# Kernel tuning notes

Measured on AMD Instinct MI355X. Metric: run time of the kernel, lower is better.

## Reference

```python
import jax, jax.numpy as jnp
import numpy as np

T, B, C = 2048, 8, 1024
H, K, PAD_L = 16, 31, 30
G = C // H


def setup_inputs() -> dict:
    key = jax.random.key(0)
    k1, k2 = jax.random.split(key)
    x = jax.random.normal(k1, (T, B, C), dtype=jnp.float32)
    # xavier_uniform for weight of shape (H, 1, K): fan_in=K, fan_out=H*... torch treats
    # dims as (out=H, in=1, receptive=K) -> fan_in=1*K, fan_out=H? Actually torch computes
    # fan_in = 1*K, fan_out = H*K for a (H,1,K) tensor is not right; torch: fan_in = in*rf = 1*K,
    # fan_out = out*rf = H*K? No: for (H,1,K), fan_in = 1*K, fan_out = H*K / H? Use standard formula:
    # fan_in = size(1)*K = K, fan_out = size(0)*K = H*K -> bound = sqrt(6/(K + H*K))
    bound = float(np.sqrt(6.0 / (K + H * K)))
    weight = jax.random.uniform(k2, (H, 1, K), dtype=jnp.float32, minval=-bound, maxval=bound)
    bias = jnp.zeros((C,), dtype=jnp.float32)
    return {"x": x, "weight": weight, "bias": bias}


def reference(x, weight, bias):
    # x: [T, B, C]; weight: [H, 1, K]; bias: [C]
    w = jax.nn.softmax(weight, axis=-1)  # per-head softmax over kernel taps
    # expand head weights to per-channel depthwise kernel: [C, 1, K]
    w_ch = jnp.repeat(w, G, axis=0)  # each of the G channels in head h shares w[h]
    xb = jnp.transpose(x, (1, 2, 0))  # [B, C, T]
    out = jax.lax.conv_general_dilated(
        xb, w_ch,
        window_strides=(1,),
        padding=[(PAD_L, 0)],  # left (causal) padding
        dimension_numbers=("NCH", "OIH", "NCH"),
        feature_group_count=C,
    )  # [B, C, T]
    out = jnp.transpose(out, (2, 0, 1))  # [T, B, C]
    return out + bias
```

## Files before the change

kernel.cpp:

```cpp
#include <hip/hip_runtime.h>
#include <hip/hip_bf16.h>

constexpr int T = 2048;
constexpr int B = 8;
constexpr int C = 1024;
constexpr int H = 16;
constexpr int K = 31;
constexpr int BC = B * C;

constexpr int TT = 32;
constexpr int NB = K - 1 + TT;
constexpr int BLOCK = 256;
constexpr int BLK_PER_CHUNK = BC / BLOCK;
constexpr int NCHUNK = T / TT;
constexpr int NBLK = BLK_PER_CHUNK * NCHUNK;

__global__ __launch_bounds__(BLOCK, 4) void lconv_tbc_kernel(
        const float* __restrict__ x,
        const float* __restrict__ w,
        const float* __restrict__ bias,
        float* __restrict__ out) {
    const int tid = threadIdx.x;
    const int cb = blockIdx.x & (BLK_PER_CHUNK - 1);
    const int chunk = blockIdx.x / BLK_PER_CHUNK;
    const int bc = cb * BLOCK + tid;
    const int c = bc & (C - 1);
    const int h = __builtin_amdgcn_readfirstlane(c >> 6);

    float wv[K];
    float m = -1e30f;
    #pragma unroll
    for (int k = 0; k < K; ++k) {
        wv[k] = w[h * K + k];
        m = fmaxf(m, wv[k]);
    }
    float s = 0.0f;
    #pragma unroll
    for (int k = 0; k < K; ++k) {
        wv[k] = __expf(wv[k] - m);
        s += wv[k];
    }
    const float inv = 1.0f / s;
    float wr[K];
    #pragma unroll
    for (int d = 0; d < K; ++d)
        wr[d] = __uint_as_float(
            __builtin_amdgcn_readfirstlane(__float_as_uint(wv[K - 1 - d] * inv)));

    const float bi = bias[c];
    const int t0 = chunk * TT;
    const int base = t0 * BC + bc;

    float buf[NB];
    if (chunk == 0) {
        #pragma unroll
        for (int j = 0; j < K - 1; ++j) buf[j] = 0.0f;
    } else {
        #pragma unroll
        for (int j = 0; j < K - 1; ++j)
            buf[j] = x[base + (j - (K - 1)) * BC];
    }
    #pragma unroll
    for (int u = 0; u < TT; ++u)
        buf[K - 1 + u] = x[base + u * BC];

    #pragma unroll
    for (int u = 0; u < TT; ++u) {
        float acc = bi;
        #pragma unroll
        for (int d = 0; d < K; ++d)
            acc = fmaf(wr[d], buf[K - 1 + u - d], acc);
        __builtin_nontemporal_store(acc, &out[base + u * BC]);
    }
}

extern "C" void kernel_launch(void* const* d_in, const int* in_sizes, int n_in,
                              void* d_out, int out_size, void* d_ws, size_t ws_size,
                              hipStream_t stream) {
    const float* x = (const float*)d_in[0];
    const float* w = (const float*)d_in[1];
    const float* bias = (const float*)d_in[2];
    float* out = (float*)d_out;

    lconv_tbc_kernel<<<dim3(NBLK), dim3(BLOCK), 0, stream>>>(x, w, bias, out);
}
```

Before: 29.97 us.

## Stage input tile into LDS via async global_load_lds before convolution

Replaces the per-thread scalar global loads of the 61-row time window with wave-cooperative 16-byte global_load_lds transfers into a shared tile, overlapped with the softmax weight computation, then reads rows from LDS into registers after a barrier. It aims to cut the number of memory instructions and hide load latency behind the softmax. In exchange it adds about 61KB of LDS per block plus a block-wide sync, and lowers the launch-bounds occupancy hint from 4 to 2.

```diff
diff --git a/kernel.cpp b/kernel.cpp
--- a/kernel.cpp
+++ b/kernel.cpp
@@ -1,5 +1,5 @@
 #include <hip/hip_runtime.h>
-#include <hip/hip_bf16.h>
+#include <stdint.h>
 
 constexpr int T = 2048;
 constexpr int B = 8;
@@ -9,23 +9,44 @@
 constexpr int BC = B * C;
 
 constexpr int TT = 32;
-constexpr int NB = K - 1 + TT;
+constexpr int NR = K - 1 + TT;
 constexpr int BLOCK = 256;
 constexpr int BLK_PER_CHUNK = BC / BLOCK;
 constexpr int NCHUNK = T / TT;
 constexpr int NBLK = BLK_PER_CHUNK * NCHUNK;
 
-__global__ __launch_bounds__(BLOCK, 4) void lconv_tbc_kernel(
+typedef const __attribute__((address_space(1))) uint32_t gas_u32;
+typedef __attribute__((address_space(3))) uint32_t las_u32;
+
+__global__ __launch_bounds__(BLOCK, 2) void lconv_tbc_kernel(
         const float* __restrict__ x,
         const float* __restrict__ w,
         const float* __restrict__ bias,
         float* __restrict__ out) {
+    __shared__ float tile[NR][BLOCK];
+
     const int tid = threadIdx.x;
+    const int wid = tid >> 6;
+    const int lane = tid & 63;
     const int cb = blockIdx.x & (BLK_PER_CHUNK - 1);
     const int chunk = blockIdx.x / BLK_PER_CHUNK;
-    const int bc = cb * BLOCK + tid;
+    const int bc0 = cb * BLOCK;
+    const int bc = bc0 + tid;
     const int c = bc & (C - 1);
     const int h = __builtin_amdgcn_readfirstlane(c >> 6);
+    const int t0 = chunk * TT;
+
+    for (int r = wid; r < NR; r += 4) {
+        const int tg = t0 - (K - 1) + r;
+        if (tg >= 0) {
+            const float* src = x + (size_t)tg * BC + bc0 + lane * 4;
+            __builtin_amdgcn_global_load_lds(
+                (gas_u32*)src, (las_u32*)&tile[r][lane * 4], 16, 0, 0);
+        } else {
+            float4 z = {0.f, 0.f, 0.f, 0.f};
+            *(float4*)&tile[r][lane * 4] = z;
+        }
+    }
 
     float wv[K];
     float m = -1e30f;
@@ -46,24 +67,15 @@
     for (int d = 0; d < K; ++d)
         wr[d] = __uint_as_float(
             __builtin_amdgcn_readfirstlane(__float_as_uint(wv[K - 1 - d] * inv)));
+    const float bi = bias[c];
 
-    const float bi = bias[c];
-    const int t0 = chunk * TT;
+    __syncthreads();
+
+    float buf[NR];
+    #pragma unroll
+    for (int r = 0; r < NR; ++r) buf[r] = tile[r][tid];
+
     const int base = t0 * BC + bc;
-
-    float buf[NB];
-    if (chunk == 0) {
-        #pragma unroll
-        for (int j = 0; j < K - 1; ++j) buf[j] = 0.0f;
-    } else {
-        #pragma unroll
-        for (int j = 0; j < K - 1; ++j)
-            buf[j] = x[base + (j - (K - 1)) * BC];
-    }
-    #pragma unroll
-    for (int u = 0; u < TT; ++u)
-        buf[K - 1 + u] = x[base + u * BC];
-
     #pragma unroll
     for (int u = 0; u < TT; ++u) {
         float acc = bi;
```

Measured after the change: 31.32 us. +4.5%, slower.

## Double-buffer input chunks via async global-to-LDS loads with register halo reuse

Applied to the files above, without the earlier changes.

Each block now processes a 64-step time segment in four 16-step chunks. The next chunk is streamed into a double-buffered LDS area with global_load_lds DMA while the current chunk is computed, and hand-written vmcnt waits sequence the two. The 30-step halo is carried in registers between chunks, which cuts the redundant halo reloads of the old one-chunk-per-block scheme from about 1x to about 0.5x of the input. In exchange it relies on fragile hard-coded vmcnt counts that also count the stores, uses more LDS, and launches fewer blocks.

```diff
diff --git a/kernel.cpp b/kernel.cpp
--- a/kernel.cpp
+++ b/kernel.cpp
@@ -1,5 +1,5 @@
 #include <hip/hip_runtime.h>
-#include <hip/hip_bf16.h>
+#include <stdint.h>
 
 constexpr int T = 2048;
 constexpr int B = 8;
@@ -7,25 +7,40 @@
 constexpr int H = 16;
 constexpr int K = 31;
 constexpr int BC = B * C;
+constexpr int HALO = K - 1;
 
-constexpr int TT = 32;
-constexpr int NB = K - 1 + TT;
+constexpr int TT = 16;
+constexpr int NCH = 4;
+constexpr int SEG = TT * NCH;
 constexpr int BLOCK = 256;
-constexpr int BLK_PER_CHUNK = BC / BLOCK;
-constexpr int NCHUNK = T / TT;
-constexpr int NBLK = BLK_PER_CHUNK * NCHUNK;
+constexpr int NSLICE = BC / BLOCK;
+constexpr int NSEG = T / SEG;
+constexpr int NBLK = NSLICE * NSEG;
+
+constexpr int DMA_PER_CHUNK = TT / 4;
+static_assert(DMA_PER_CHUNK == 4, "vmcnt literals below assume 4 DMA/chunk");
+static_assert(TT == 16, "vmcnt literals below assume 16 stores/chunk");
+
+typedef const __attribute__((address_space(1))) uint32_t gas_u32;
+typedef __attribute__((address_space(3))) uint32_t las_u32;
 
 __global__ __launch_bounds__(BLOCK, 4) void lconv_tbc_kernel(
         const float* __restrict__ x,
         const float* __restrict__ w,
         const float* __restrict__ bias,
         float* __restrict__ out) {
+    __shared__ float lds[4][2][TT][64];
+
     const int tid = threadIdx.x;
-    const int cb = blockIdx.x & (BLK_PER_CHUNK - 1);
-    const int chunk = blockIdx.x / BLK_PER_CHUNK;
-    const int bc = cb * BLOCK + tid;
+    const int wid = tid >> 6;
+    const int lane = tid & 63;
+    const int slice = blockIdx.x & (NSLICE - 1);
+    const int seg = blockIdx.x >> 5;
+    const int bc0w = slice * BLOCK + wid * 64;
+    const int bc = bc0w + lane;
     const int c = bc & (C - 1);
     const int h = __builtin_amdgcn_readfirstlane(c >> 6);
+    const int ts0 = seg * SEG;
 
     float wv[K];
     float m = -1e30f;
@@ -46,31 +61,68 @@
     for (int d = 0; d < K; ++d)
         wr[d] = __uint_as_float(
             __builtin_amdgcn_readfirstlane(__float_as_uint(wv[K - 1 - d] * inv)));
+    const float bi = bias[c];
 
-    const float bi = bias[c];
-    const int t0 = chunk * TT;
-    const int base = t0 * BC + bc;
-
-    float buf[NB];
-    if (chunk == 0) {
+    float halo[HALO];
+    if (seg == 0) {
         #pragma unroll
-        for (int j = 0; j < K - 1; ++j) buf[j] = 0.0f;
+        for (int j = 0; j < HALO; ++j) halo[j] = 0.0f;
     } else {
         #pragma unroll
-        for (int j = 0; j < K - 1; ++j)
-            buf[j] = x[base + (j - (K - 1)) * BC];
+        for (int j = 0; j < HALO; ++j)
+            halo[j] = x[(ts0 - HALO + j) * BC + bc];
     }
-    #pragma unroll
-    for (int u = 0; u < TT; ++u)
-        buf[K - 1 + u] = x[base + u * BC];
+
+    const int dma_off = (lane >> 4) * BC + bc0w + (lane & 15) * 4;
 
     #pragma unroll
-    for (int u = 0; u < TT; ++u) {
-        float acc = bi;
+    for (int i = 0; i < DMA_PER_CHUNK; ++i)
+        __builtin_amdgcn_global_load_lds(
+            (gas_u32*)(x + (ts0 + 4 * i) * BC + dma_off),
+            (las_u32*)&lds[wid][0][4 * i][0], 16, 0, 0);
+
+    #pragma unroll
+    for (int k = 0; k < NCH; ++k) {
+        const int t0 = ts0 + k * TT;
+
+        if (k + 1 < NCH) {
+            #pragma unroll
+            for (int i = 0; i < DMA_PER_CHUNK; ++i)
+                __builtin_amdgcn_global_load_lds(
+                    (gas_u32*)(x + (t0 + TT + 4 * i) * BC + dma_off),
+                    (las_u32*)&lds[wid][(k + 1) & 1][4 * i][0], 16, 0, 0);
+        }
+
+        if (k == 0)           asm volatile("s_waitcnt vmcnt(4)" ::: "memory");
+        else if (k + 1 < NCH) asm volatile("s_waitcnt vmcnt(20)" ::: "memory");
+        else                  asm volatile("s_waitcnt vmcnt(16)" ::: "memory");
+
+        float cur[TT];
         #pragma unroll
-        for (int d = 0; d < K; ++d)
-            acc = fmaf(wr[d], buf[K - 1 + u - d], acc);
-        __builtin_nontemporal_store(acc, &out[base + u * BC]);
+        for (int r = 0; r < TT; ++r) cur[r] = lds[wid][k & 1][r][lane];
+
+        #pragma unroll
+        for (int u = 0; u < TT; ++u) {
+            float acc = bi;
+            #pragma unroll
+            for (int d = 0; d < K; ++d) {
+                const int j = u - d;
+                const float v = (j >= 0) ? cur[j] : halo[HALO + j];
+                acc = fmaf(wr[d], v, acc);
+            }
+            __builtin_nontemporal_store(acc, &out[(t0 + u) * BC + bc]);
+        }
+
+        if (k + 1 < NCH) {
+            float nh[HALO];
+            #pragma unroll
+            for (int j = 0; j < HALO; ++j) {
+                const int tj = j - (HALO - TT);
+                nh[j] = (tj >= 0) ? cur[tj] : halo[j + TT];
+            }
+            #pragma unroll
+            for (int j = 0; j < HALO; ++j) halo[j] = nh[j];
+        }
     }
 }
 
```

New measurement: 35.73 us. +19.2%, slower.
